# Kernel tuning notes

Hardware: AMD Instinct MI355X
Metric: run time of the kernel (lower is better)

Reference implementation:

```python
import jax, jax.numpy as jnp
import jax.lax as lax
import numpy as np

B, T, I, HS = 32, 2048, 256, 256
H = HS // 2  # per-direction hidden (hidden_size even -> fwd/bwd both H)


def setup_inputs() -> dict:
    key = jax.random.key(0)
    ks = jax.random.split(key, 10)
    s = 1.0 / np.sqrt(H)
    u = lambda k, shape: jax.random.uniform(k, shape, jnp.float32, -s, s)
    x = jax.random.normal(ks[0], (B, T, I), jnp.float32)
    lengths = jax.random.randint(ks[1], (B,), 1, T + 1)
    return {
        "x": x,
        "lengths": lengths,
        "Wf_ih": u(ks[2], (4 * H, I)), "Wf_hh": u(ks[3], (4 * H, H)),
        "bf_ih": u(ks[4], (4 * H,)), "bf_hh": u(ks[5], (4 * H,)),
        "Wb_ih": u(ks[6], (4 * H, I)), "Wb_hh": u(ks[7], (4 * H, H)),
        "bb_ih": u(ks[8], (4 * H,)), "bb_hh": u(ks[9], (4 * H,)),
    }


def _lstm_scan(x_seq, W_ih, W_hh, b_ih, b_hh):
    # x_seq: [B, T, I] -> hidden states per step [B, T, H]
    xg = jnp.einsum('bti,gi->btg', x_seq, W_ih) + b_ih  # input gates precomputed

    def step(carry, xg_t):
        h, c = carry
        gates = xg_t + h @ W_hh.T + b_hh  # [B, 4H]
        i, f, g, o = jnp.split(gates, 4, axis=-1)
        c = jax.nn.sigmoid(f) * c + jax.nn.sigmoid(i) * jnp.tanh(g)
        h = jax.nn.sigmoid(o) * jnp.tanh(c)
        return (h, c), h

    b, hdim = x_seq.shape[0], W_hh.shape[1]
    init = (jnp.zeros((b, hdim), x_seq.dtype), jnp.zeros((b, hdim), x_seq.dtype))
    _, hs = lax.scan(step, init, jnp.swapaxes(xg, 0, 1))  # [T, B, H]
    return jnp.swapaxes(hs, 0, 1)


def _flip_padded_seq(x, lengths):
    # reverse the first `length` steps of each sequence, keep padding in place
    t = jnp.arange(x.shape[1])[None, :]
    L = lengths[:, None]
    idx = jnp.where(t < L, L - 1 - t, t)  # [B, T]
    return jnp.take_along_axis(x, idx[:, :, None], axis=1)


def reference(x, lengths, Wf_ih, Wf_hh, bf_ih, bf_hh, Wb_ih, Wb_hh, bb_ih, bb_hh):
    fwd = _lstm_scan(x, Wf_ih, Wf_hh, bf_ih, bf_hh)
    x_rev = _flip_padded_seq(x, lengths)
    bwd = _lstm_scan(x_rev, Wb_ih, Wb_hh, bb_ih, bb_hh)
    return jnp.concatenate([fwd, bwd], axis=-1)  # [B, T, hidden_size]
```

## Files before the change

kernel.cpp:

```cpp
#include <hip/hip_runtime.h>
#include <hip/hip_fp16.h>

#define B_  32
#define T_  2048
#define I_  256
#define H_  128

typedef _Float16 f16;
typedef _Float16 f16x2 __attribute__((ext_vector_type(2)));
typedef _Float16 f16x4 __attribute__((ext_vector_type(4)));
typedef _Float16 f16x8 __attribute__((ext_vector_type(8)));
typedef float    f32x4 __attribute__((ext_vector_type(4)));

#if __has_builtin(__builtin_amdgcn_fdot2)
#define FDOT2(a, b, c) __builtin_amdgcn_fdot2((a), (b), (c), false)
#else
static __device__ __forceinline__ float FDOT2(f16x2 a, f16x2 b, float c) {
  return c + (float)a[0] * (float)b[0] + (float)a[1] * (float)b[1];
}
#endif

static __device__ __forceinline__ f16x2 asf16x2(unsigned u) {
  return __builtin_bit_cast(f16x2, u);
}

#define DPPF(x, ctrl)                                                      \
  __builtin_bit_cast(float, __builtin_amdgcn_mov_dpp(                      \
      __builtin_bit_cast(int, (x)), (ctrl), 0xF, 0xF, true))

static __device__ __forceinline__ float fast_sig(float x) {
  float e = __builtin_amdgcn_exp2f(-1.44269504089f * x);
  return __builtin_amdgcn_rcpf(1.0f + e);
}
static __device__ __forceinline__ float fast_tanh(float x) {
  float e = __builtin_amdgcn_exp2f(-2.88539008178f * x);
  return 2.0f * __builtin_amdgcn_rcpf(1.0f + e) - 1.0f;
}

#define BARRIER_LDS()                                   \
  __builtin_amdgcn_sched_barrier(0);                    \
  asm volatile("s_waitcnt lgkmcnt(0)" ::: "memory");    \
  __builtin_amdgcn_s_barrier();                         \
  __builtin_amdgcn_sched_barrier(0)

#define MFMA16(a, b, c) __builtin_amdgcn_mfma_f32_16x16x32_f16((a), (b), (c), 0, 0, 0)

__global__ __launch_bounds__(256) void xg_gemm(
    const float* __restrict__ x,
    const float* __restrict__ Wf, const float* __restrict__ Wb,
    const float* __restrict__ bf_ih, const float* __restrict__ bf_hh,
    const float* __restrict__ bb_ih, const float* __restrict__ bb_hh,
    f16* __restrict__ xg)
{
  __shared__ f16 xs[128][136];
  __shared__ f16 wt[128][136];

  const int tid = threadIdx.x;
  const int m0  = blockIdx.y * 128;
  const int n0  = blockIdx.x * 128;

  const float* Wsrc; const float* bih; const float* bhh; int nb; size_t dbase;
  if (n0 < 512) { Wsrc = Wf; bih = bf_ih; bhh = bf_hh; nb = n0;       dbase = 0; }
  else          { Wsrc = Wb; bih = bb_ih; bhh = bb_hh; nb = n0 - 512; dbase = 512; }

  const int w  = tid >> 6;
  const int l  = tid & 63;
  const int lr = l & 15;
  const int lk = (l >> 4) * 8;

  f32x4 acc[2][8] = {};

  #pragma unroll
  for (int kh = 0; kh < 2; ++kh) {
    #pragma unroll
    for (int it = 0; it < 16; ++it) {
      int idx = it * 256 + tid;
      int row = idx >> 5, c4 = idx & 31;
      float4 v = *(const float4*)&x[(size_t)(m0 + row) * I_ + kh * 128 + c4 * 4];
      f16x4 h4 = { (f16)v.x, (f16)v.y, (f16)v.z, (f16)v.w };
      *(f16x4*)&xs[row][c4 * 4] = h4;
    }
    #pragma unroll
    for (int it = 0; it < 16; ++it) {
      int idx = it * 256 + tid;
      int row = idx >> 5, c4 = idx & 31;
      float4 v = *(const float4*)&Wsrc[(size_t)(nb + row) * I_ + kh * 128 + c4 * 4];
      f16x4 h4 = { (f16)v.x, (f16)v.y, (f16)v.z, (f16)v.w };
      *(f16x4*)&wt[row][c4 * 4] = h4;
    }
    __syncthreads();

    #pragma unroll
    for (int ks = 0; ks < 4; ++ks) {
      int kk = ks * 32 + lk;
      f16x8 a0 = *(const f16x8*)&xs[w * 32 + lr][kk];
      f16x8 a1 = *(const f16x8*)&xs[w * 32 + 16 + lr][kk];
      #pragma unroll
      for (int nt = 0; nt < 8; ++nt) {
        f16x8 bf = *(const f16x8*)&wt[nt * 16 + lr][kk];
        acc[0][nt] = MFMA16(a0, bf, acc[0][nt]);
        acc[1][nt] = MFMA16(a1, bf, acc[1][nt]);
      }
    }
    __syncthreads();
  }

  #pragma unroll
  for (int mt = 0; mt < 2; ++mt) {
    #pragma unroll
    for (int nt = 0; nt < 8; ++nt) {
      int nloc = nt * 16 + lr;
      int grow = nb + nloc;
      int gate = grow >> 7, unit = grow & 127;
      size_t col = dbase + (size_t)unit * 4 + gate;
      float bias = bih[grow] + bhh[grow];
      #pragma unroll
      for (int r = 0; r < 4; ++r) {
        int m = m0 + w * 32 + mt * 16 + (l >> 4) * 4 + r;
        xg[(size_t)m * 1024 + col] = (f16)(acc[mt][nt][r] + bias);
      }
    }
  }
}

__global__ __launch_bounds__(512, 1) void birnn_rec(
    const f16* __restrict__ xg,
    const float* __restrict__ Wfhh, const float* __restrict__ Wbhh,
    const int* __restrict__ lengths,
    float* __restrict__ out)
{
  const int tid = threadIdx.x;
  const int w   = tid >> 6;
  const int l   = tid & 63;
  const int sl  = (l & 3) | ((l >> 5) << 2);
  const int g   = w * 8 + ((l >> 2) & 7);
  const int r   = g * 8 + sl;
  const int uu  = r >> 2;
  const int gg  = r & 3;
  const int dir = blockIdx.x >> 5;
  const int b   = blockIdx.x & 31;
  const float* Whh = dir ? Wbhh : Wfhh;
  const int L   = lengths[b];

  unsigned wrg[8][8];
  #pragma unroll
  for (int j = 0; j < 8; ++j) {
    int lrow = g * 8 + (j ^ sl);
    const float* src = &Whh[(size_t)((lrow & 3) * 128 + (lrow >> 2)) * H_ + sl * 16];
    #pragma unroll
    for (int k4 = 0; k4 < 4; ++k4) {
      float4 v = *(const float4*)&src[k4 * 4];
      wrg[j][2 * k4]     = __builtin_bit_cast(unsigned, (f16x2){ (f16)v.x, (f16)v.y });
      wrg[j][2 * k4 + 1] = __builtin_bit_cast(unsigned, (f16x2){ (f16)v.z, (f16)v.w });
    }
  }

  __shared__ __align__(16) f16 hbuf[2][128];
  if (tid < 128) hbuf[0][tid] = (f16)0.0f;
  float c = 0.0f;
  __syncthreads();

  auto rowof = [&](int t) -> size_t {
    int it = t;
    if (dir) it = (t < L) ? (L - 1 - t) : t;
    return (size_t)(b * T_ + it) * 1024 + (size_t)dir * 512 + (size_t)r;
  };

  f16 pa = xg[rowof(0)];
  f16 pb = xg[rowof(1)];

  const float bscale = (gg == 2) ? 2.0f : 1.0f;
  const float bmul   = (gg == 2) ? 2.0f : 1.0f;
  const float badd   = (gg == 2) ? -1.0f : 0.0f;
  const bool  writer = (gg == 0);

#define STEP(t, P, RB, WB)                                                   \
  {                                                                          \
    float xv = (float)(P);                                                   \
    if ((t) + 2 < T_) P = xg[rowof((t) + 2)];                                \
    uint4 hA = *(const uint4*)&hbuf[RB][sl * 16];                            \
    uint4 hB = *(const uint4*)&hbuf[RB][sl * 16 + 8];                        \
    float p[8] = { 0.f, 0.f, 0.f, 0.f, 0.f, 0.f, 0.f, 0.f };                 \
    _Pragma("unroll")                                                        \
    for (int j = 0; j < 8; ++j) {                                            \
      p[j] = FDOT2(asf16x2(hA.x), asf16x2(wrg[j][0]), p[j]);                 \
      p[j] = FDOT2(asf16x2(hA.y), asf16x2(wrg[j][1]), p[j]);                 \
      p[j] = FDOT2(asf16x2(hA.z), asf16x2(wrg[j][2]), p[j]);                 \
      p[j] = FDOT2(asf16x2(hA.w), asf16x2(wrg[j][3]), p[j]);                 \
      p[j] = FDOT2(asf16x2(hB.x), asf16x2(wrg[j][4]), p[j]);                 \
      p[j] = FDOT2(asf16x2(hB.y), asf16x2(wrg[j][5]), p[j]);                 \
      p[j] = FDOT2(asf16x2(hB.z), asf16x2(wrg[j][6]), p[j]);                 \
      p[j] = FDOT2(asf16x2(hB.w), asf16x2(wrg[j][7]), p[j]);                 \
    }                                                                        \
        \
    p[0] += DPPF(p[1], 0xB1);                                                \
    p[2] += DPPF(p[3], 0xB1);                                                \
    p[4] += DPPF(p[5], 0xB1);                                                \
    p[6] += DPPF(p[7], 0xB1);                                                \
    p[0] += DPPF(p[2], 0x4E);                                                \
    p[4] += DPPF(p[6], 0x4E);                                                \
    p[0] += __shfl_xor(p[4], 32, 64);                                        \
    float sum = p[0] + xv;                                                   \
    float act = fast_sig(bscale * sum) * bmul + badd;                        \
          \
    float a1 = DPPF(act, 0xB1);                                              \
    float a2 = DPPF(act, 0x4E);                                              \
    float a3 = DPPF(act, 0x1B);                                              \
          \
    c = a1 * c + act * a2;                                                   \
    float hval = a3 * fast_tanh(c);                                          \
    if (writer) {                                                            \
      hbuf[WB][uu] = (f16)hval;                                              \
      out[(size_t)(b * T_ + (t)) * 256 + dir * 128 + uu] = hval;             \
    }                                                                        \
    BARRIER_LDS();                                                           \
  }

  for (int tt = 0; tt < T_; tt += 2) {
    STEP(tt,     pa, 0, 1)
    STEP(tt + 1, pb, 1, 0)
  }
#undef STEP
}

extern "C" void kernel_launch(void* const* d_in, const int* in_sizes, int n_in,
                              void* d_out, int out_size, void* d_ws, size_t ws_size,
                              hipStream_t stream) {
  const float* x      = (const float*)d_in[0];
  const int*   lengths= (const int*)  d_in[1];
  const float* Wf_ih  = (const float*)d_in[2];
  const float* Wf_hh  = (const float*)d_in[3];
  const float* bf_ih  = (const float*)d_in[4];
  const float* bf_hh  = (const float*)d_in[5];
  const float* Wb_ih  = (const float*)d_in[6];
  const float* Wb_hh  = (const float*)d_in[7];
  const float* bb_ih  = (const float*)d_in[8];
  const float* bb_hh  = (const float*)d_in[9];
  float* out = (float*)d_out;
  f16*   xg  = (f16*)d_ws;

  (void)in_sizes; (void)n_in; (void)out_size; (void)ws_size;

  xg_gemm<<<dim3(8, 512), 256, 0, stream>>>(x, Wf_ih, Wb_ih,
                                            bf_ih, bf_hh, bb_ih, bb_hh, xg);
  birnn_rec<<<dim3(64), 512, 0, stream>>>(xg, Wf_hh, Wb_hh, lengths, out);
}
```

Before: 1.220 ms.

## Process two batch sequences per workgroup in recurrent LSTM kernel

Each workgroup now runs the recurrence for two batch elements at once, reusing the register-resident W_hh weights for both and interleaving their independent dot products and activation chains within one barrier per step. The grid shrinks from 64 to 32 workgroups. The aim is to hide the serial latency of each step (LDS reads, DPP reductions, barrier) through instruction-level parallelism across two independent chains, at the cost of half as many CUs being used and roughly twice the work per step.

```diff
diff --git a/kernel.cpp b/kernel.cpp
--- a/kernel.cpp
+++ b/kernel.cpp
@@ -137,10 +137,13 @@
   const int r   = g * 8 + sl;
   const int uu  = r >> 2;
   const int gg  = r & 3;
-  const int dir = blockIdx.x >> 5;
-  const int b   = blockIdx.x & 31;
+  const int wg  = blockIdx.x;
+  const int dir = wg >> 4;
+  const int bA  = (wg & 15) * 2;
+  const int bB  = bA + 1;
   const float* Whh = dir ? Wbhh : Wfhh;
-  const int L   = lengths[b];
+  const int LA  = lengths[bA];
+  const int LB  = lengths[bB];
 
   unsigned wrg[8][8];
   #pragma unroll
@@ -155,72 +158,91 @@
     }
   }
 
-  __shared__ __align__(16) f16 hbuf[2][128];
-  if (tid < 128) hbuf[0][tid] = (f16)0.0f;
-  float c = 0.0f;
+  __shared__ __align__(16) f16 hbufA[2][128];
+  __shared__ __align__(16) f16 hbufB[2][128];
+  if (tid < 128) { hbufA[0][tid] = (f16)0.0f; hbufB[0][tid] = (f16)0.0f; }
+  float cA = 0.0f, cB = 0.0f;
   __syncthreads();
 
-  auto rowof = [&](int t) -> size_t {
+  auto rowofA = [&](int t) -> size_t {
     int it = t;
-    if (dir) it = (t < L) ? (L - 1 - t) : t;
-    return (size_t)(b * T_ + it) * 1024 + (size_t)dir * 512 + (size_t)r;
+    if (dir) it = (t < LA) ? (LA - 1 - t) : t;
+    return (size_t)(bA * T_ + it) * 1024 + (size_t)dir * 512 + (size_t)r;
   };
-
-  f16 pa = xg[rowof(0)];
-  f16 pb = xg[rowof(1)];
+  auto rowofB = [&](int t) -> size_t {
+    int it = t;
+    if (dir) it = (t < LB) ? (LB - 1 - t) : t;
+    return (size_t)(bB * T_ + it) * 1024 + (size_t)dir * 512 + (size_t)r;
+  };
+
+  f16 paA = xg[rowofA(0)], pbA = xg[rowofA(1)];
+  f16 paB = xg[rowofB(0)], pbB = xg[rowofB(1)];
 
   const float bscale = (gg == 2) ? 2.0f : 1.0f;
   const float bmul   = (gg == 2) ? 2.0f : 1.0f;
   const float badd   = (gg == 2) ? -1.0f : 0.0f;
   const bool  writer = (gg == 0);
 
-#define STEP(t, P, RB, WB)                                                   \
-  {                                                                          \
-    float xv = (float)(P);                                                   \
-    if ((t) + 2 < T_) P = xg[rowof((t) + 2)];                                \
-    uint4 hA = *(const uint4*)&hbuf[RB][sl * 16];                            \
-    uint4 hB = *(const uint4*)&hbuf[RB][sl * 16 + 8];                        \
-    float p[8] = { 0.f, 0.f, 0.f, 0.f, 0.f, 0.f, 0.f, 0.f };                 \
+#define DOTS(hbuf, RB, P)                                                    \
+    uint4 hA_##P = *(const uint4*)&hbuf[RB][sl * 16];                        \
+    uint4 hB_##P = *(const uint4*)&hbuf[RB][sl * 16 + 8];                    \
+    float P[8] = { 0.f, 0.f, 0.f, 0.f, 0.f, 0.f, 0.f, 0.f };                 \
     _Pragma("unroll")                                                        \
     for (int j = 0; j < 8; ++j) {                                            \
-      p[j] = FDOT2(asf16x2(hA.x), asf16x2(wrg[j][0]), p[j]);                 \
-      p[j] = FDOT2(asf16x2(hA.y), asf16x2(wrg[j][1]), p[j]);                 \
-      p[j] = FDOT2(asf16x2(hA.z), asf16x2(wrg[j][2]), p[j]);                 \
-      p[j] = FDOT2(asf16x2(hA.w), asf16x2(wrg[j][3]), p[j]);                 \
-      p[j] = FDOT2(asf16x2(hB.x), asf16x2(wrg[j][4]), p[j]);                 \
-      p[j] = FDOT2(asf16x2(hB.y), asf16x2(wrg[j][5]), p[j]);                 \
-      p[j] = FDOT2(asf16x2(hB.z), asf16x2(wrg[j][6]), p[j]);                 \
-      p[j] = FDOT2(asf16x2(hB.w), asf16x2(wrg[j][7]), p[j]);                 \
-    }                                                                        \
-        \
-    p[0] += DPPF(p[1], 0xB1);                                                \
-    p[2] += DPPF(p[3], 0xB1);                                                \
-    p[4] += DPPF(p[5], 0xB1);                                                \
-    p[6] += DPPF(p[7], 0xB1);                                                \
-    p[0] += DPPF(p[2], 0x4E);                                                \
-    p[4] += DPPF(p[6], 0x4E);                                                \
-    p[0] += __shfl_xor(p[4], 32, 64);                                        \
-    float sum = p[0] + xv;                                                   \
+      P[j] = FDOT2(asf16x2(hA_##P.x), asf16x2(wrg[j][0]), P[j]);             \
+      P[j] = FDOT2(asf16x2(hA_##P.y), asf16x2(wrg[j][1]), P[j]);             \
+      P[j] = FDOT2(asf16x2(hA_##P.z), asf16x2(wrg[j][2]), P[j]);             \
+      P[j] = FDOT2(asf16x2(hA_##P.w), asf16x2(wrg[j][3]), P[j]);             \
+      P[j] = FDOT2(asf16x2(hB_##P.x), asf16x2(wrg[j][4]), P[j]);             \
+      P[j] = FDOT2(asf16x2(hB_##P.y), asf16x2(wrg[j][5]), P[j]);             \
+      P[j] = FDOT2(asf16x2(hB_##P.z), asf16x2(wrg[j][6]), P[j]);             \
+      P[j] = FDOT2(asf16x2(hB_##P.w), asf16x2(wrg[j][7]), P[j]);             \
+    }
+
+#define FINISH(P, xv, cS, hbuf, WB, bX, t)                                   \
+  {                                                                          \
+    P[0] += DPPF(P[1], 0xB1);                                                \
+    P[2] += DPPF(P[3], 0xB1);                                                \
+    P[4] += DPPF(P[5], 0xB1);                                                \
+    P[6] += DPPF(P[7], 0xB1);                                                \
+    P[0] += DPPF(P[2], 0x4E);                                                \
+    P[4] += DPPF(P[6], 0x4E);                                                \
+    P[0] += __shfl_xor(P[4], 32, 64);                                        \
+    float sum = P[0] + (xv);                                                 \
     float act = fast_sig(bscale * sum) * bmul + badd;                        \
-          \
     float a1 = DPPF(act, 0xB1);                                              \
     float a2 = DPPF(act, 0x4E);                                              \
     float a3 = DPPF(act, 0x1B);                                              \
-          \
-    c = a1 * c + act * a2;                                                   \
-    float hval = a3 * fast_tanh(c);                                          \
+    cS = a1 * cS + act * a2;                                                 \
+    float hval = a3 * fast_tanh(cS);                                         \
     if (writer) {                                                            \
       hbuf[WB][uu] = (f16)hval;                                              \
-      out[(size_t)(b * T_ + (t)) * 256 + dir * 128 + uu] = hval;             \
+      out[(size_t)((bX) * T_ + (t)) * 256 + dir * 128 + uu] = hval;          \
     }                                                                        \
+  }
+
+#define STEP2(t, PA, PB, RB, WB)                                             \
+  {                                                                          \
+    float xvA = (float)(PA);                                                 \
+    float xvB = (float)(PB);                                                 \
+    if ((t) + 2 < T_) {                                                      \
+      PA = xg[rowofA((t) + 2)];                                              \
+      PB = xg[rowofB((t) + 2)];                                              \
+    }                                                                        \
+    DOTS(hbufA, RB, pA)                                                      \
+    DOTS(hbufB, RB, pB)                                                      \
+    FINISH(pA, xvA, cA, hbufA, WB, bA, t)                                    \
+    FINISH(pB, xvB, cB, hbufB, WB, bB, t)                                    \
     BARRIER_LDS();                                                           \
   }
 
   for (int tt = 0; tt < T_; tt += 2) {
-    STEP(tt,     pa, 0, 1)
-    STEP(tt + 1, pb, 1, 0)
-  }
-#undef STEP
+    STEP2(tt,     paA, paB, 0, 1)
+    STEP2(tt + 1, pbA, pbB, 1, 0)
+  }
+#undef STEP2
+#undef FINISH
+#undef DOTS
 }
 
 extern "C" void kernel_launch(void* const* d_in, const int* in_sizes, int n_in,
@@ -243,5 +265,5 @@
 
   xg_gemm<<<dim3(8, 512), 256, 0, stream>>>(x, Wf_ih, Wb_ih,
                                             bf_ih, bf_hh, bb_ih, bb_hh, xg);
-  birnn_rec<<<dim3(64), 512, 0, stream>>>(xg, Wf_hh, Wb_hh, lengths, out);
-}
+  birnn_rec<<<dim3(32), 512, 0, stream>>>(xg, Wf_hh, Wb_hh, lengths, out);
+}
```

Measured after the change: 2.100 ms. 72.2% more time.

## Fuse input-gate GEMM into recurrent kernel with chunked ring-buffer pipeline

Applied to the files above, without the earlier changes.

Removes the separate full-size xg GEMM and its large fp16 intermediate. Each recurrent block now computes its own input-gate projections two chunks ahead with MFMA, interleaved with the per-step recurrence, and writes them to a small per-block ring buffer in workspace. x tiles are staged a further chunk ahead through triple-buffered LDS, and W_ih is pre-converted to fp16 in gate-interleaved order by a small prep kernel. The aim is to hide the GEMM inside the latency-bound recurrence, at the cost of extra per-step instructions and a vmcnt barrier per chunk on the critical path.

```diff
diff --git a/kernel.cpp b/kernel.cpp
--- a/kernel.cpp
+++ b/kernel.cpp
@@ -5,6 +5,8 @@
 #define T_  2048
 #define I_  256
 #define H_  128
+#define CH_ 16
+#define NCH (T_ / CH_)
 
 typedef _Float16 f16;
 typedef _Float16 f16x2 __attribute__((ext_vector_type(2)));
@@ -45,89 +47,27 @@
 
 #define MFMA16(a, b, c) __builtin_amdgcn_mfma_f32_16x16x32_f16((a), (b), (c), 0, 0, 0)
 
-__global__ __launch_bounds__(256) void xg_gemm(
-    const float* __restrict__ x,
-    const float* __restrict__ Wf, const float* __restrict__ Wb,
+__global__ __launch_bounds__(64) void wprep(
+    const float* __restrict__ Wf_ih, const float* __restrict__ Wb_ih,
+    f16* __restrict__ wih16)
+{
+  int row = blockIdx.x;
+  int d = row >> 9, col = row & 511;
+  int unit = col >> 2, gate = col & 3;
+  const float* src = (d ? Wb_ih : Wf_ih) + (size_t)(gate * 128 + unit) * I_;
+  int t = threadIdx.x;
+  float4 v = *(const float4*)&src[t * 4];
+  f16x4 h = { (f16)v.x, (f16)v.y, (f16)v.z, (f16)v.w };
+  *(f16x4*)&wih16[(size_t)row * I_ + t * 4] = h;
+}
+
+__global__ __launch_bounds__(512, 1) void birnn_fused(
+    const float* __restrict__ x, const f16* __restrict__ wih,
+    const float* __restrict__ Wfhh, const float* __restrict__ Wbhh,
     const float* __restrict__ bf_ih, const float* __restrict__ bf_hh,
     const float* __restrict__ bb_ih, const float* __restrict__ bb_hh,
-    f16* __restrict__ xg)
-{
-  __shared__ f16 xs[128][136];
-  __shared__ f16 wt[128][136];
-
-  const int tid = threadIdx.x;
-  const int m0  = blockIdx.y * 128;
-  const int n0  = blockIdx.x * 128;
-
-  const float* Wsrc; const float* bih; const float* bhh; int nb; size_t dbase;
-  if (n0 < 512) { Wsrc = Wf; bih = bf_ih; bhh = bf_hh; nb = n0;       dbase = 0; }
-  else          { Wsrc = Wb; bih = bb_ih; bhh = bb_hh; nb = n0 - 512; dbase = 512; }
-
-  const int w  = tid >> 6;
-  const int l  = tid & 63;
-  const int lr = l & 15;
-  const int lk = (l >> 4) * 8;
-
-  f32x4 acc[2][8] = {};
-
-  #pragma unroll
-  for (int kh = 0; kh < 2; ++kh) {
-    #pragma unroll
-    for (int it = 0; it < 16; ++it) {
-      int idx = it * 256 + tid;
-      int row = idx >> 5, c4 = idx & 31;
-      float4 v = *(const float4*)&x[(size_t)(m0 + row) * I_ + kh * 128 + c4 * 4];
-      f16x4 h4 = { (f16)v.x, (f16)v.y, (f16)v.z, (f16)v.w };
-      *(f16x4*)&xs[row][c4 * 4] = h4;
-    }
-    #pragma unroll
-    for (int it = 0; it < 16; ++it) {
-      int idx = it * 256 + tid;
-      int row = idx >> 5, c4 = idx & 31;
-      float4 v = *(const float4*)&Wsrc[(size_t)(nb + row) * I_ + kh * 128 + c4 * 4];
-      f16x4 h4 = { (f16)v.x, (f16)v.y, (f16)v.z, (f16)v.w };
-      *(f16x4*)&wt[row][c4 * 4] = h4;
-    }
-    __syncthreads();
-
-    #pragma unroll
-    for (int ks = 0; ks < 4; ++ks) {
-      int kk = ks * 32 + lk;
-      f16x8 a0 = *(const f16x8*)&xs[w * 32 + lr][kk];
-      f16x8 a1 = *(const f16x8*)&xs[w * 32 + 16 + lr][kk];
-      #pragma unroll
-      for (int nt = 0; nt < 8; ++nt) {
-        f16x8 bf = *(const f16x8*)&wt[nt * 16 + lr][kk];
-        acc[0][nt] = MFMA16(a0, bf, acc[0][nt]);
-        acc[1][nt] = MFMA16(a1, bf, acc[1][nt]);
-      }
-    }
-    __syncthreads();
-  }
-
-  #pragma unroll
-  for (int mt = 0; mt < 2; ++mt) {
-    #pragma unroll
-    for (int nt = 0; nt < 8; ++nt) {
-      int nloc = nt * 16 + lr;
-      int grow = nb + nloc;
-      int gate = grow >> 7, unit = grow & 127;
-      size_t col = dbase + (size_t)unit * 4 + gate;
-      float bias = bih[grow] + bhh[grow];
-      #pragma unroll
-      for (int r = 0; r < 4; ++r) {
-        int m = m0 + w * 32 + mt * 16 + (l >> 4) * 4 + r;
-        xg[(size_t)m * 1024 + col] = (f16)(acc[mt][nt][r] + bias);
-      }
-    }
-  }
-}
-
-__global__ __launch_bounds__(512, 1) void birnn_rec(
-    const f16* __restrict__ xg,
-    const float* __restrict__ Wfhh, const float* __restrict__ Wbhh,
-    const int* __restrict__ lengths,
-    float* __restrict__ out)
+    const int* __restrict__ lengths, float* __restrict__ out,
+    f16* __restrict__ xgring)
 {
   const int tid = threadIdx.x;
   const int w   = tid >> 6;
@@ -137,6 +77,8 @@
   const int r   = g * 8 + sl;
   const int uu  = r >> 2;
   const int gg  = r & 3;
+  const int a_row = l & 15;
+  const int koff  = (l >> 4) * 8;
   const int dir = blockIdx.x >> 5;
   const int b   = blockIdx.x & 31;
   const float* Whh = dir ? Wbhh : Wfhh;
@@ -155,31 +97,123 @@
     }
   }
 
+  const float* bih_ = dir ? bb_ih : bf_ih;
+  const float* bhh_ = dir ? bb_hh : bf_hh;
+  float biasv[4];
+  #pragma unroll
+  for (int nt = 0; nt < 4; ++nt) {
+    int ncol = w * 64 + nt * 16 + a_row;
+    int grow = (ncol & 3) * 128 + (ncol >> 2);
+    biasv[nt] = bih_[grow] + bhh_[grow];
+  }
+
+  __shared__ __align__(16) f16 xb[3][16][264];
   __shared__ __align__(16) f16 hbuf[2][128];
+
+  const size_t ringbase = (size_t)(dir * 32 + b) * 64 * 512;
+  const f32x4 ZED = { 0.f, 0.f, 0.f, 0.f };
+
+  auto stagex = [&](int chunk, int slot) {
+    int xr = tid >> 5, c8 = (tid & 31) * 8;
+    int t3 = chunk * CH_ + xr;
+    int it3 = dir ? ((t3 < L) ? (L - 1 - t3) : t3) : t3;
+    const float* xs_ = &x[(size_t)(b * T_ + it3) * I_ + c8];
+    float4 va = *(const float4*)xs_;
+    float4 vb = *(const float4*)(xs_ + 4);
+    f16x8 hv = { (f16)va.x, (f16)va.y, (f16)va.z, (f16)va.w,
+                 (f16)vb.x, (f16)vb.y, (f16)vb.z, (f16)vb.w };
+    *(f16x8*)&xb[slot][xr][c8] = hv;
+  };
+
+  auto produce = [&](int chunk, int slot) {
+    f32x4 e0, e1, e2, e3;
+    #pragma unroll
+    for (int kc = 0; kc < 8; ++kc) {
+      f16x8 af = *(const f16x8*)&xb[slot][a_row][kc * 32 + koff];
+      const f16* wb_ = wih + (size_t)(dir * 512 + w * 64 + a_row) * 256 + kc * 32 + koff;
+      f16x8 q0 = *(const f16x8*)(wb_);
+      f16x8 q1 = *(const f16x8*)(wb_ + 4096);
+      f16x8 q2 = *(const f16x8*)(wb_ + 8192);
+      f16x8 q3 = *(const f16x8*)(wb_ + 12288);
+      if (kc == 0) { e0 = MFMA16(af, q0, ZED); e1 = MFMA16(af, q1, ZED);
+                     e2 = MFMA16(af, q2, ZED); e3 = MFMA16(af, q3, ZED); }
+      else         { e0 = MFMA16(af, q0, e0);  e1 = MFMA16(af, q1, e1);
+                     e2 = MFMA16(af, q2, e2);  e3 = MFMA16(af, q3, e3);  }
+    }
+    #pragma unroll
+    for (int i = 0; i < 16; ++i) {
+      float val = ((i < 4) ? e0[i & 3] : (i < 8) ? e1[i & 3]
+                  : (i < 12) ? e2[i & 3] : e3[i & 3]) + biasv[i >> 2];
+      int s_out = (l >> 4) * 4 + (i & 3);
+      int t_out = chunk * CH_ + s_out;
+      int col   = w * 64 + (i >> 2) * 16 + a_row;
+      xgring[ringbase + (size_t)(t_out & 63) * 512 + col] = (f16)val;
+    }
+  };
+
+  stagex(0, 0); stagex(1, 1); stagex(2, 2);
+  __syncthreads();
+  produce(0, 0); produce(1, 1);
+  __builtin_amdgcn_sched_barrier(0);
+  asm volatile("s_waitcnt vmcnt(0)" ::: "memory");
+  __syncthreads();
   if (tid < 128) hbuf[0][tid] = (f16)0.0f;
   float c = 0.0f;
   __syncthreads();
 
-  auto rowof = [&](int t) -> size_t {
-    int it = t;
-    if (dir) it = (t < L) ? (L - 1 - t) : t;
-    return (size_t)(b * T_ + it) * 1024 + (size_t)dir * 512 + (size_t)r;
-  };
-
-  f16 pa = xg[rowof(0)];
-  f16 pb = xg[rowof(1)];
+  f16 pa = xgring[ringbase + 0 * 512 + r];
+  f16 pb = xgring[ringbase + 1 * 512 + r];
 
   const float bscale = (gg == 2) ? 2.0f : 1.0f;
   const float bmul   = (gg == 2) ? 2.0f : 1.0f;
   const float badd   = (gg == 2) ? -1.0f : 0.0f;
   const bool  writer = (gg == 0);
 
-#define STEP(t, P, RB, WB)                                                   \
+#define STEPF(s, P)                                                          \
   {                                                                          \
+    const int t = cc * CH_ + (s);                                            \
     float xv = (float)(P);                                                   \
-    if ((t) + 2 < T_) P = xg[rowof((t) + 2)];                                \
-    uint4 hA = *(const uint4*)&hbuf[RB][sl * 16];                            \
-    uint4 hB = *(const uint4*)&hbuf[RB][sl * 16 + 8];                        \
+    if (t + 2 < T_) P = xgring[ringbase + (size_t)((t + 2) & 63) * 512 + r]; \
+    if (prod && (s) < 8) {                                                   \
+      f16x8 af = *(const f16x8*)&xb[xread][a_row][(s) * 32 + koff];          \
+      const f16* wb_ = wih + (size_t)(dir * 512 + w * 64 + a_row) * 256      \
+                       + (s) * 32 + koff;                                    \
+      f16x8 q0 = *(const f16x8*)(wb_);                                       \
+      f16x8 q1 = *(const f16x8*)(wb_ + 4096);                                \
+      f16x8 q2 = *(const f16x8*)(wb_ + 8192);                                \
+      f16x8 q3 = *(const f16x8*)(wb_ + 12288);                               \
+      if ((s) == 0) { d0 = MFMA16(af, q0, ZED); d1 = MFMA16(af, q1, ZED);    \
+                      d2 = MFMA16(af, q2, ZED); d3 = MFMA16(af, q3, ZED); }  \
+      else          { d0 = MFMA16(af, q0, d0);  d1 = MFMA16(af, q1, d1);     \
+                      d2 = MFMA16(af, q2, d2);  d3 = MFMA16(af, q3, d3);  }  \
+    }                                                                        \
+    if (prod && (s) >= 8) {                                                  \
+      _Pragma("unroll")                                                      \
+      for (int e = 0; e < 2; ++e) {                                          \
+        int i = ((s) - 8) * 2 + e;                                           \
+        float val = ((i < 4) ? d0[i & 3] : (i < 8) ? d1[i & 3]               \
+                    : (i < 12) ? d2[i & 3] : d3[i & 3]) + biasv[i >> 2];     \
+        int s_out = (l >> 4) * 4 + (i & 3);                                  \
+        int t_out = (cc + 2) * CH_ + s_out;                                  \
+        int col   = w * 64 + (i >> 2) * 16 + a_row;                          \
+        xgring[ringbase + (size_t)(t_out & 63) * 512 + col] = (f16)val;      \
+      }                                                                      \
+    }                                                                        \
+    if (xload && (s) == 4) {                                                 \
+      int xr = tid >> 5, c8 = (tid & 31) * 8;                                \
+      int t3 = (cc + 3) * CH_ + xr;                                          \
+      int it3 = dir ? ((t3 < L) ? (L - 1 - t3) : t3) : t3;                   \
+      const float* xs_ = &x[(size_t)(b * T_ + it3) * I_ + c8];               \
+      xva = *(const float4*)xs_;                                             \
+      xvb = *(const float4*)(xs_ + 4);                                       \
+    }                                                                        \
+    if (xload && (s) == 14) {                                                \
+      f16x8 hv = { (f16)xva.x, (f16)xva.y, (f16)xva.z, (f16)xva.w,           \
+                   (f16)xvb.x, (f16)xvb.y, (f16)xvb.z, (f16)xvb.w };         \
+      *(f16x8*)&xb[xwrit][tid >> 5][(tid & 31) * 8] = hv;                    \
+    }                                                                        \
+    uint4 hA = *(const uint4*)&hbuf[(s) & 1][sl * 16];                       \
+    uint4 hB = *(const uint4*)&hbuf[(s) & 1][sl * 16 + 8];                   \
     float p[8] = { 0.f, 0.f, 0.f, 0.f, 0.f, 0.f, 0.f, 0.f };                 \
     _Pragma("unroll")                                                        \
     for (int j = 0; j < 8; ++j) {                                            \
@@ -192,7 +226,6 @@
       p[j] = FDOT2(asf16x2(hB.z), asf16x2(wrg[j][6]), p[j]);                 \
       p[j] = FDOT2(asf16x2(hB.w), asf16x2(wrg[j][7]), p[j]);                 \
     }                                                                        \
-        \
     p[0] += DPPF(p[1], 0xB1);                                                \
     p[2] += DPPF(p[3], 0xB1);                                                \
     p[4] += DPPF(p[5], 0xB1);                                                \
@@ -202,25 +235,40 @@
     p[0] += __shfl_xor(p[4], 32, 64);                                        \
     float sum = p[0] + xv;                                                   \
     float act = fast_sig(bscale * sum) * bmul + badd;                        \
-          \
     float a1 = DPPF(act, 0xB1);                                              \
     float a2 = DPPF(act, 0x4E);                                              \
     float a3 = DPPF(act, 0x1B);                                              \
-          \
     c = a1 * c + act * a2;                                                   \
     float hval = a3 * fast_tanh(c);                                          \
     if (writer) {                                                            \
-      hbuf[WB][uu] = (f16)hval;                                              \
-      out[(size_t)(b * T_ + (t)) * 256 + dir * 128 + uu] = hval;             \
+      hbuf[((s) & 1) ^ 1][uu] = (f16)hval;                                   \
+      out[(size_t)(b * T_ + t) * 256 + dir * 128 + uu] = hval;               \
     }                                                                        \
     BARRIER_LDS();                                                           \
   }
 
-  for (int tt = 0; tt < T_; tt += 2) {
-    STEP(tt,     pa, 0, 1)
-    STEP(tt + 1, pb, 1, 0)
-  }
-#undef STEP
+  for (int cc = 0; cc < NCH; ++cc) {
+    const int  xread = (cc + 2) % 3;
+    const int  xwrit = (cc + 3) % 3;
+    const bool prod  = (cc + 2) < NCH;
+    const bool xload = (cc + 3) < NCH;
+    f32x4 d0, d1, d2, d3;
+    float4 xva, xvb;
+
+    #pragma unroll
+    for (int s = 0; s < CH_; s += 2) {
+      STEPF(s,     pa)
+      STEPF(s + 1, pb)
+    }
+
+    if (prod) {
+      __builtin_amdgcn_sched_barrier(0);
+      asm volatile("s_waitcnt vmcnt(0)" ::: "memory");
+      __builtin_amdgcn_s_barrier();
+      __builtin_amdgcn_sched_barrier(0);
+    }
+  }
+#undef STEPF
 }
 
 extern "C" void kernel_launch(void* const* d_in, const int* in_sizes, int n_in,
@@ -237,11 +285,14 @@
   const float* bb_ih  = (const float*)d_in[8];
   const float* bb_hh  = (const float*)d_in[9];
   float* out = (float*)d_out;
-  f16*   xg  = (f16*)d_ws;
+
+  f16* wih16  = (f16*)d_ws;
+  f16* xgring = (f16*)d_ws + 2 * 512 * 256;
 
   (void)in_sizes; (void)n_in; (void)out_size; (void)ws_size;
 
-  xg_gemm<<<dim3(8, 512), 256, 0, stream>>>(x, Wf_ih, Wb_ih,
-                                            bf_ih, bf_hh, bb_ih, bb_hh, xg);
-  birnn_rec<<<dim3(64), 512, 0, stream>>>(xg, Wf_hh, Wb_hh, lengths, out);
-}
+  wprep<<<dim3(1024), 64, 0, stream>>>(Wf_ih, Wb_ih, wih16);
+  birnn_fused<<<dim3(64), 512, 0, stream>>>(x, wih16, Wf_hh, Wb_hh,
+                                            bf_ih, bf_hh, bb_ih, bb_hh,
+                                            lengths, out, xgring);
+}
```

Result: slower. 1.914 ms (+57.0%).
